# Kernel tuning notes

Measured on AMD Instinct MI355X. Metric: run time of the kernel, lower is better.

Reference implementation:

```python
import jax, jax.numpy as jnp
import numpy as np

N_ATOMS = 1536
FEAT = 32
N_GAUSS = 16
N_TYPES = 10
CUTOFF = 5.0
CELL = 30.0  # orthorhombic box edge (cell_diag)
GAMMA = 10.0


def setup_inputs() -> dict:
    key = jax.random.key(0)
    ks = jax.random.split(key, 8)
    xyz = jax.random.uniform(ks[0], (N_ATOMS, 3), dtype=jnp.float32) * CELL
    z = jax.random.randint(ks[1], (N_ATOMS,), 0, N_TYPES)
    emb = jax.random.normal(ks[2], (N_TYPES, FEAT), dtype=jnp.float32) * 0.1
    W1 = jax.random.normal(ks[3], (N_GAUSS, FEAT), dtype=jnp.float32) * 0.1
    b1 = jnp.zeros((FEAT,), jnp.float32)
    W2 = jax.random.normal(ks[4], (FEAT, FEAT), dtype=jnp.float32) * 0.1
    b2 = jnp.zeros((FEAT,), jnp.float32)
    W3 = jax.random.normal(ks[5], (FEAT, 1), dtype=jnp.float32) * 0.1
    b3 = jnp.zeros((1,), jnp.float32)
    return {"xyz": xyz, "z": z, "emb": emb, "W1": W1, "b1": b1,
            "W2": W2, "b2": b2, "W3": W3, "b3": b3}


def reference(xyz, z, emb, W1, b1, W2, b2, W3, b3):
    # --- generate_nbr_list: pairwise displacement + minimum-image PBC wrap ---
    disp = xyz[None, :, :] - xyz[:, None, :]              # [N,N,3]
    shift = (disp < -0.5 * CELL).astype(jnp.float32) - (disp >= 0.5 * CELL).astype(jnp.float32)
    disp = disp + shift * CELL                            # wrapped offsets applied
    d2 = jnp.sum(disp * disp, axis=-1)                    # [N,N]
    mask = (d2 < CUTOFF * CUTOFF) & (d2 > 0.0)            # cutoff neighbor mask, no self
    d = jnp.sqrt(jnp.where(mask, d2, 1.0))                # safe sqrt
    # --- SchNet-like GNN energy on the masked neighbor structure ---
    mu = jnp.linspace(0.0, CUTOFF, N_GAUSS, dtype=jnp.float32)
    rbf = jnp.exp(-GAMMA * (d[..., None] - mu) ** 2) * mask[..., None]  # [N,N,G]
    filt = jnp.tanh(rbf @ W1 + b1) * mask[..., None]      # [N,N,F]
    h = emb[z]                                            # [N,F] atom embeddings
    agg = jnp.einsum('ijf,jf->if', filt, h)               # message aggregation
    u = jax.nn.silu((h + agg) @ W2 + b2)                  # atomwise readout
    e_atom = u @ W3 + b3                                  # [N,1]
    return jnp.sum(e_atom)                                # total energy (scalar)
```

## Files before the change

### kernel.cpp

```cpp
#include <hip/hip_runtime.h>

#define N_ATOMS  1536
#define FEAT     32
#define N_GAUSS  16
#define MAXNBR   128

__global__ __launch_bounds__(64) void gnn_atom_kernel(
    const float* __restrict__ xyz, const int* __restrict__ z,
    const float* __restrict__ emb, const float* __restrict__ W1,
    const float* __restrict__ b1,  const float* __restrict__ W2,
    const float* __restrict__ b2,  const float* __restrict__ W3,
    float* __restrict__ e_atom)
{
    const int i   = blockIdx.x;
    const int tid = threadIdx.x;

    __shared__ int   s_nbr[MAXNBR];
    __shared__ float s_dist[MAXNBR];
    __shared__ float s_x[FEAT];
    __shared__ int   s_cnt;

    if (tid == 0) s_cnt = 0;
    __syncthreads();

    const float xi = xyz[3*i+0], yi = xyz[3*i+1], zi = xyz[3*i+2];

    for (int j = tid; j < N_ATOMS; j += 64) {
        float dx = xyz[3*j+0] - xi;
        float dy = xyz[3*j+1] - yi;
        float dz = xyz[3*j+2] - zi;
        dx += (dx < -15.0f ? 30.0f : 0.0f) - (dx >= 15.0f ? 30.0f : 0.0f);
        dy += (dy < -15.0f ? 30.0f : 0.0f) - (dy >= 15.0f ? 30.0f : 0.0f);
        dz += (dz < -15.0f ? 30.0f : 0.0f) - (dz >= 15.0f ? 30.0f : 0.0f);
        float d2 = dx*dx + dy*dy + dz*dz;
        if (d2 < 25.0f && d2 > 0.0f) {
            int slot = atomicAdd(&s_cnt, 1);
            if (slot < MAXNBR) { s_nbr[slot] = j; s_dist[slot] = sqrtf(d2); }
        }
    }
    __syncthreads();
    const int cnt = min(s_cnt, MAXNBR);

    const int fl   = tid & 7;
    const int slot = tid >> 3;
    const float4 b1v = *(const float4*)&b1[fl*4];
    float af[4] = {0.0f, 0.0f, 0.0f, 0.0f};

    for (int p = slot; p < cnt; p += 8) {
        const int   j  = s_nbr[p];
        const float d  = s_dist[p];
        const int   zj = z[j];
        float s0 = b1v.x, s1 = b1v.y, s2 = b1v.z, s3 = b1v.w;
        #pragma unroll
        for (int g = 0; g < N_GAUSS; ++g) {
            float t = d - (float)g * (5.0f / 15.0f);
            float r = __expf(-10.0f * t * t);
            const float4 w = *(const float4*)&W1[g * FEAT + fl * 4];
            s0 = fmaf(r, w.x, s0); s1 = fmaf(r, w.y, s1);
            s2 = fmaf(r, w.z, s2); s3 = fmaf(r, w.w, s3);
        }
        const float4 hj = *(const float4*)&emb[zj * FEAT + fl * 4];
        float sv[4] = {s0, s1, s2, s3};
        float hv[4] = {hj.x, hj.y, hj.z, hj.w};
        #pragma unroll
        for (int ff = 0; ff < 4; ++ff) {
            float t2 = __expf(-2.0f * fabsf(sv[ff]));
            float th = copysignf((1.0f - t2) / (1.0f + t2), sv[ff]);
            af[ff] = fmaf(th, hv[ff], af[ff]);
        }
    }

    #pragma unroll
    for (int ff = 0; ff < 4; ++ff) {
        af[ff] += __shfl_xor(af[ff], 8,  64);
        af[ff] += __shfl_xor(af[ff], 16, 64);
        af[ff] += __shfl_xor(af[ff], 32, 64);
    }

    if (tid < 8) {
        const float4 hi = *(const float4*)&emb[z[i] * FEAT + tid * 4];
        s_x[tid*4+0] = af[0] + hi.x;
        s_x[tid*4+1] = af[1] + hi.y;
        s_x[tid*4+2] = af[2] + hi.z;
        s_x[tid*4+3] = af[3] + hi.w;
    }
    __syncthreads();

    float e = 0.0f;
    if (tid < FEAT) {
        float s = b2[tid];
        #pragma unroll
        for (int k = 0; k < FEAT; ++k)
            s = fmaf(s_x[k], W2[k * FEAT + tid], s);
        float u = s / (1.0f + __expf(-s));
        e = u * W3[tid];
    }
    e += __shfl_xor(e, 16, 64);
    e += __shfl_xor(e, 8,  64);
    e += __shfl_xor(e, 4,  64);
    e += __shfl_xor(e, 2,  64);
    e += __shfl_xor(e, 1,  64);
    if (tid == 0) e_atom[i] = e;
}

__global__ __launch_bounds__(256) void gnn_sum_kernel(
    const float* __restrict__ e_atom, const float* __restrict__ b3,
    float* __restrict__ out)
{
    const int tid = threadIdx.x;
    float s = 0.0f;
    #pragma unroll
    for (int k = 0; k < N_ATOMS / 256; ++k) s += e_atom[tid + k * 256];
    #pragma unroll
    for (int off = 32; off > 0; off >>= 1)
        s += __shfl_xor(s, off, 64);
    __shared__ float r[4];
    if ((tid & 63) == 0) r[tid >> 6] = s;
    __syncthreads();
    if (tid == 0)
        out[0] = r[0] + r[1] + r[2] + r[3] + (float)N_ATOMS * b3[0];
}

extern "C" void kernel_launch(void* const* d_in, const int* in_sizes, int n_in,
                              void* d_out, int out_size, void* d_ws, size_t ws_size,
                              hipStream_t stream) {
    const float* xyz = (const float*)d_in[0];
    const int*   z   = (const int*)  d_in[1];
    const float* emb = (const float*)d_in[2];
    const float* W1  = (const float*)d_in[3];
    const float* b1  = (const float*)d_in[4];
    const float* W2  = (const float*)d_in[5];
    const float* b2  = (const float*)d_in[6];
    const float* W3  = (const float*)d_in[7];
    const float* b3  = (const float*)d_in[8];
    float* out    = (float*)d_out;
    float* e_atom = (float*)d_ws;

    gnn_atom_kernel<<<N_ATOMS, 64, 0, stream>>>(xyz, z, emb, W1, b1, W2, b2, W3, e_atom);
    gnn_sum_kernel<<<1, 256, 0, stream>>>(e_atom, b3, out);
}
```

Before: 20.50 us.

## Fuse atom and sum kernels with last-block reduction, four atoms per block

Each 256-thread block now handles four atoms, one per wavefront. Every xyz[j] load in the neighbor scan is reused for all four atoms. The separate reduction kernel is removed: an atomic counter picks the last block to finish, and that block sums the per-atom energies. The trade-off is an extra hipMemsetAsync per launch and a quarter as many blocks, with more shared-memory atomics per block.

```diff
diff --git a/kernel.cpp b/kernel.cpp
--- a/kernel.cpp
+++ b/kernel.cpp
@@ -4,60 +4,77 @@
 #define FEAT     32
 #define N_GAUSS  16
 #define MAXNBR   128
+#define APB      4
+#define NBLK     (N_ATOMS / APB)
+#define NTHREADS 256
 
-__global__ __launch_bounds__(64) void gnn_atom_kernel(
+__global__ __launch_bounds__(NTHREADS) void gnn_fused_kernel(
     const float* __restrict__ xyz, const int* __restrict__ z,
     const float* __restrict__ emb, const float* __restrict__ W1,
     const float* __restrict__ b1,  const float* __restrict__ W2,
     const float* __restrict__ b2,  const float* __restrict__ W3,
-    float* __restrict__ e_atom)
+    const float* __restrict__ b3,
+    float* __restrict__ e_atom, int* __restrict__ counter,
+    float* __restrict__ out)
 {
-    const int i   = blockIdx.x;
-    const int tid = threadIdx.x;
+    const int tid  = threadIdx.x;
+    const int lane = tid & 63;
+    const int w    = tid >> 6;
+    const int a0   = blockIdx.x * APB;
 
-    __shared__ int   s_nbr[MAXNBR];
-    __shared__ float s_dist[MAXNBR];
-    __shared__ float s_x[FEAT];
-    __shared__ int   s_cnt;
+    __shared__ float s_px[APB], s_py[APB], s_pz[APB];
+    __shared__ int   s_nbr[APB][MAXNBR];
+    __shared__ float s_dist[APB][MAXNBR];
+    __shared__ float s_x[APB][FEAT];
+    __shared__ int   s_cnt[APB];
+    __shared__ int   s_last;
+    __shared__ float s_red[4];
 
-    if (tid == 0) s_cnt = 0;
+    if (tid < APB) {
+        s_cnt[tid] = 0;
+        s_px[tid] = xyz[3*(a0+tid)+0];
+        s_py[tid] = xyz[3*(a0+tid)+1];
+        s_pz[tid] = xyz[3*(a0+tid)+2];
+    }
     __syncthreads();
 
-    const float xi = xyz[3*i+0], yi = xyz[3*i+1], zi = xyz[3*i+2];
-
-    for (int j = tid; j < N_ATOMS; j += 64) {
-        float dx = xyz[3*j+0] - xi;
-        float dy = xyz[3*j+1] - yi;
-        float dz = xyz[3*j+2] - zi;
-        dx += (dx < -15.0f ? 30.0f : 0.0f) - (dx >= 15.0f ? 30.0f : 0.0f);
-        dy += (dy < -15.0f ? 30.0f : 0.0f) - (dy >= 15.0f ? 30.0f : 0.0f);
-        dz += (dz < -15.0f ? 30.0f : 0.0f) - (dz >= 15.0f ? 30.0f : 0.0f);
-        float d2 = dx*dx + dy*dy + dz*dz;
-        if (d2 < 25.0f && d2 > 0.0f) {
-            int slot = atomicAdd(&s_cnt, 1);
-            if (slot < MAXNBR) { s_nbr[slot] = j; s_dist[slot] = sqrtf(d2); }
+    for (int j = tid; j < N_ATOMS; j += NTHREADS) {
+        const float pjx = xyz[3*j+0], pjy = xyz[3*j+1], pjz = xyz[3*j+2];
+        #pragma unroll
+        for (int q = 0; q < APB; ++q) {
+            float dx = pjx - s_px[q];
+            float dy = pjy - s_py[q];
+            float dz = pjz - s_pz[q];
+            dx += (dx < -15.0f ? 30.0f : 0.0f) - (dx >= 15.0f ? 30.0f : 0.0f);
+            dy += (dy < -15.0f ? 30.0f : 0.0f) - (dy >= 15.0f ? 30.0f : 0.0f);
+            dz += (dz < -15.0f ? 30.0f : 0.0f) - (dz >= 15.0f ? 30.0f : 0.0f);
+            float d2 = dx*dx + dy*dy + dz*dz;
+            if (d2 < 25.0f && d2 > 0.0f) {
+                int slot = atomicAdd(&s_cnt[q], 1);
+                if (slot < MAXNBR) { s_nbr[q][slot] = j; s_dist[q][slot] = sqrtf(d2); }
+            }
         }
     }
     __syncthreads();
-    const int cnt = min(s_cnt, MAXNBR);
 
-    const int fl   = tid & 7;
-    const int slot = tid >> 3;
+    const int cnt  = min(s_cnt[w], MAXNBR);
+    const int fl   = lane & 7;
+    const int slot = lane >> 3;
     const float4 b1v = *(const float4*)&b1[fl*4];
     float af[4] = {0.0f, 0.0f, 0.0f, 0.0f};
 
     for (int p = slot; p < cnt; p += 8) {
-        const int   j  = s_nbr[p];
-        const float d  = s_dist[p];
+        const int   j  = s_nbr[w][p];
+        const float d  = s_dist[w][p];
         const int   zj = z[j];
         float s0 = b1v.x, s1 = b1v.y, s2 = b1v.z, s3 = b1v.w;
         #pragma unroll
         for (int g = 0; g < N_GAUSS; ++g) {
             float t = d - (float)g * (5.0f / 15.0f);
             float r = __expf(-10.0f * t * t);
-            const float4 w = *(const float4*)&W1[g * FEAT + fl * 4];
-            s0 = fmaf(r, w.x, s0); s1 = fmaf(r, w.y, s1);
-            s2 = fmaf(r, w.z, s2); s3 = fmaf(r, w.w, s3);
+            const float4 wv = *(const float4*)&W1[g * FEAT + fl * 4];
+            s0 = fmaf(r, wv.x, s0); s1 = fmaf(r, wv.y, s1);
+            s2 = fmaf(r, wv.z, s2); s3 = fmaf(r, wv.w, s3);
         }
         const float4 hj = *(const float4*)&emb[zj * FEAT + fl * 4];
         float sv[4] = {s0, s1, s2, s3};
@@ -69,56 +86,59 @@
             af[ff] = fmaf(th, hv[ff], af[ff]);
         }
     }
-
     #pragma unroll
     for (int ff = 0; ff < 4; ++ff) {
         af[ff] += __shfl_xor(af[ff], 8,  64);
         af[ff] += __shfl_xor(af[ff], 16, 64);
         af[ff] += __shfl_xor(af[ff], 32, 64);
     }
-
-    if (tid < 8) {
-        const float4 hi = *(const float4*)&emb[z[i] * FEAT + tid * 4];
-        s_x[tid*4+0] = af[0] + hi.x;
-        s_x[tid*4+1] = af[1] + hi.y;
-        s_x[tid*4+2] = af[2] + hi.z;
-        s_x[tid*4+3] = af[3] + hi.w;
+    if (lane < 8) {
+        const float4 hi = *(const float4*)&emb[z[a0 + w] * FEAT + lane * 4];
+        s_x[w][lane*4+0] = af[0] + hi.x;
+        s_x[w][lane*4+1] = af[1] + hi.y;
+        s_x[w][lane*4+2] = af[2] + hi.z;
+        s_x[w][lane*4+3] = af[3] + hi.w;
     }
     __syncthreads();
 
     float e = 0.0f;
-    if (tid < FEAT) {
-        float s = b2[tid];
+    if (lane < FEAT) {
+        float s = b2[lane];
         #pragma unroll
         for (int k = 0; k < FEAT; ++k)
-            s = fmaf(s_x[k], W2[k * FEAT + tid], s);
+            s = fmaf(s_x[w][k], W2[k * FEAT + lane], s);
         float u = s / (1.0f + __expf(-s));
-        e = u * W3[tid];
+        e = u * W3[lane];
     }
     e += __shfl_xor(e, 16, 64);
     e += __shfl_xor(e, 8,  64);
     e += __shfl_xor(e, 4,  64);
     e += __shfl_xor(e, 2,  64);
     e += __shfl_xor(e, 1,  64);
-    if (tid == 0) e_atom[i] = e;
-}
+    if (lane == 0)
+        __hip_atomic_store(&e_atom[a0 + w], e, __ATOMIC_RELAXED, __HIP_MEMORY_SCOPE_AGENT);
 
-__global__ __launch_bounds__(256) void gnn_sum_kernel(
-    const float* __restrict__ e_atom, const float* __restrict__ b3,
-    float* __restrict__ out)
-{
-    const int tid = threadIdx.x;
-    float s = 0.0f;
-    #pragma unroll
-    for (int k = 0; k < N_ATOMS / 256; ++k) s += e_atom[tid + k * 256];
-    #pragma unroll
-    for (int off = 32; off > 0; off >>= 1)
-        s += __shfl_xor(s, off, 64);
-    __shared__ float r[4];
-    if ((tid & 63) == 0) r[tid >> 6] = s;
     __syncthreads();
-    if (tid == 0)
-        out[0] = r[0] + r[1] + r[2] + r[3] + (float)N_ATOMS * b3[0];
+    if (tid == 0) {
+        int old = __hip_atomic_fetch_add(counter, 1, __ATOMIC_ACQ_REL, __HIP_MEMORY_SCOPE_AGENT);
+        s_last = (old == NBLK - 1);
+    }
+    __syncthreads();
+    if (s_last) {
+        float s = 0.0f;
+        #pragma unroll
+        for (int k = 0; k < N_ATOMS / NTHREADS; ++k)
+            s += __hip_atomic_load(&e_atom[tid + k * NTHREADS],
+                                   __ATOMIC_RELAXED, __HIP_MEMORY_SCOPE_AGENT);
+        #pragma unroll
+        for (int off = 32; off > 0; off >>= 1)
+            s += __shfl_xor(s, off, 64);
+        if (lane == 0) s_red[w] = s;
+        __syncthreads();
+        if (tid == 0)
+            out[0] = s_red[0] + s_red[1] + s_red[2] + s_red[3]
+                   + (float)N_ATOMS * b3[0];
+    }
 }
 
 extern "C" void kernel_launch(void* const* d_in, const int* in_sizes, int n_in,
@@ -133,9 +153,11 @@
     const float* b2  = (const float*)d_in[6];
     const float* W3  = (const float*)d_in[7];
     const float* b3  = (const float*)d_in[8];
-    float* out    = (float*)d_out;
-    float* e_atom = (float*)d_ws;
+    float* out     = (float*)d_out;
+    int*   counter = (int*)d_ws;
+    float* e_atom  = (float*)((char*)d_ws + 256);
 
-    gnn_atom_kernel<<<N_ATOMS, 64, 0, stream>>>(xyz, z, emb, W1, b1, W2, b2, W3, e_atom);
-    gnn_sum_kernel<<<1, 256, 0, stream>>>(e_atom, b3, out);
+    hipMemsetAsync(counter, 0, sizeof(int), stream);
+    gnn_fused_kernel<<<NBLK, NTHREADS, 0, stream>>>(
+        xyz, z, emb, W1, b1, W2, b2, W3, b3, e_atom, counter, out);
 }
```

Measured after the change: 25.90 us. 1.26x slower.

## Fuse final energy reduction into atom kernel via per-block completion flags

Applied to the files above, without the earlier changes.

Removes the separate single-block sum kernel. Each block publishes its per-atom energy plus a release flag, and block 0 spins until all flags are set, then reduces the energies and resets the flags. This saves one kernel launch and its gap, at the cost of block 0 busy-waiting while holding a CU. It also assumes the workspace flags start at zero and that all blocks eventually get scheduled, and block 0 finishes late because it is the waiter.

```diff
diff --git a/kernel.cpp b/kernel.cpp
--- a/kernel.cpp
+++ b/kernel.cpp
@@ -5,12 +5,14 @@
 #define N_GAUSS  16
 #define MAXNBR   128
 
-__global__ __launch_bounds__(64) void gnn_atom_kernel(
+__global__ __launch_bounds__(64) void gnn_fused_kernel(
     const float* __restrict__ xyz, const int* __restrict__ z,
     const float* __restrict__ emb, const float* __restrict__ W1,
     const float* __restrict__ b1,  const float* __restrict__ W2,
     const float* __restrict__ b2,  const float* __restrict__ W3,
-    float* __restrict__ e_atom)
+    const float* __restrict__ b3,
+    float* __restrict__ e_atom, int* __restrict__ flags,
+    float* __restrict__ out)
 {
     const int i   = blockIdx.x;
     const int tid = threadIdx.x;
@@ -100,25 +102,36 @@
     e += __shfl_xor(e, 4,  64);
     e += __shfl_xor(e, 2,  64);
     e += __shfl_xor(e, 1,  64);
-    if (tid == 0) e_atom[i] = e;
-}
 
-__global__ __launch_bounds__(256) void gnn_sum_kernel(
-    const float* __restrict__ e_atom, const float* __restrict__ b3,
-    float* __restrict__ out)
-{
-    const int tid = threadIdx.x;
-    float s = 0.0f;
-    #pragma unroll
-    for (int k = 0; k < N_ATOMS / 256; ++k) s += e_atom[tid + k * 256];
-    #pragma unroll
-    for (int off = 32; off > 0; off >>= 1)
-        s += __shfl_xor(s, off, 64);
-    __shared__ float r[4];
-    if ((tid & 63) == 0) r[tid >> 6] = s;
-    __syncthreads();
-    if (tid == 0)
-        out[0] = r[0] + r[1] + r[2] + r[3] + (float)N_ATOMS * b3[0];
+    if (tid == 0) {
+        __hip_atomic_store(&e_atom[i], e, __ATOMIC_RELAXED, __HIP_MEMORY_SCOPE_AGENT);
+        __hip_atomic_store(&flags[i], 1, __ATOMIC_RELEASE, __HIP_MEMORY_SCOPE_AGENT);
+    }
+
+    if (i == 0) {
+        for (;;) {
+            bool mine = true;
+            #pragma unroll
+            for (int k = 0; k < N_ATOMS / 64; ++k)
+                mine &= (__hip_atomic_load(&flags[tid + k * 64],
+                         __ATOMIC_ACQUIRE, __HIP_MEMORY_SCOPE_AGENT) == 1);
+            if (__all(mine)) break;
+            __builtin_amdgcn_s_sleep(2);
+        }
+        float s = 0.0f;
+        #pragma unroll
+        for (int k = 0; k < N_ATOMS / 64; ++k)
+            s += __hip_atomic_load(&e_atom[tid + k * 64],
+                                   __ATOMIC_RELAXED, __HIP_MEMORY_SCOPE_AGENT);
+        #pragma unroll
+        for (int off = 32; off > 0; off >>= 1)
+            s += __shfl_xor(s, off, 64);
+        if (tid == 0) out[0] = s + (float)N_ATOMS * b3[0];
+        #pragma unroll
+        for (int k = 0; k < N_ATOMS / 64; ++k)
+            __hip_atomic_store(&flags[tid + k * 64], 0,
+                               __ATOMIC_RELAXED, __HIP_MEMORY_SCOPE_AGENT);
+    }
 }
 
 extern "C" void kernel_launch(void* const* d_in, const int* in_sizes, int n_in,
@@ -135,7 +148,8 @@
     const float* b3  = (const float*)d_in[8];
     float* out    = (float*)d_out;
     float* e_atom = (float*)d_ws;
+    int*   flags  = (int*)((char*)d_ws + 8192);
 
-    gnn_atom_kernel<<<N_ATOMS, 64, 0, stream>>>(xyz, z, emb, W1, b1, W2, b2, W3, e_atom);
-    gnn_sum_kernel<<<1, 256, 0, stream>>>(e_atom, b3, out);
+    gnn_fused_kernel<<<N_ATOMS, 64, 0, stream>>>(
+        xyz, z, emb, W1, b1, W2, b2, W3, b3, e_atom, flags, out);
 }
```

New measurement: 33.20 us. +62.0%, slower.
